# Optimization experiments

Measured on AMD Instinct MI355X. Metric: run time of the kernel, lower is better.

The kernel has to match this reference:

```python
import jax, jax.numpy as jnp
import numpy as np

B, S, D, H = 4, 2048, 1024, 16  # batch, seq, n_embd, n_head
HD = D // H  # head size = 64


def setup_inputs() -> dict:
    key = jax.random.key(0)
    ks = jax.random.split(key, 5)
    s = 0.02
    return {
        "x": jax.random.normal(ks[0], (B, S, D), dtype=jnp.float32),
        "W_attn": jax.random.normal(ks[1], (D, 3 * D), dtype=jnp.float32) * s,
        "b_attn": jnp.zeros((3 * D,), dtype=jnp.float32),
        "W_proj": jax.random.normal(ks[2], (D, D), dtype=jnp.float32) * s,
        "b_proj": jnp.zeros((D,), dtype=jnp.float32),
    }


def reference(x, W_attn, b_attn, W_proj, b_proj):
    Bx, Sx, Dx = x.shape
    qkv = x @ W_attn + b_attn  # [B,S,3D]
    q, k, v = jnp.split(qkv, 3, axis=-1)
    # [B,H,S,hd]
    q = q.reshape(Bx, Sx, H, HD).transpose(0, 2, 1, 3)
    k = k.reshape(Bx, Sx, H, HD).transpose(0, 2, 1, 3)
    v = v.reshape(Bx, Sx, H, HD).transpose(0, 2, 1, 3)
    scale = 1.0 / jnp.sqrt(jnp.asarray(HD, dtype=x.dtype))
    att = jnp.einsum("bhqd,bhkd->bhqk", q, k) * scale  # [B,H,S,S]
    causal = jnp.tril(jnp.ones((Sx, Sx), dtype=bool))
    att = jnp.where(causal[None, None, :, :], att, jnp.asarray(-jnp.inf, dtype=att.dtype))
    att = jax.nn.softmax(att, axis=-1)
    y = jnp.einsum("bhqk,bhkd->bhqd", att, v)  # [B,H,S,hd]
    y = y.transpose(0, 2, 1, 3).reshape(Bx, Sx, Dx)
    return y @ W_proj + b_proj
```

## Files before the change

### kernel.cpp

```cpp
#include <hip/hip_runtime.h>
#include <math.h>

#define SEQ 2048
#define DIM 1024
#define NH 16
#define HD 64
#define QKV_LD 3072

typedef __attribute__((ext_vector_type(8))) __bf16 bf16x8;
typedef __attribute__((ext_vector_type(8))) unsigned short u16x8;
typedef __attribute__((ext_vector_type(4))) unsigned short u16x4;
typedef __attribute__((ext_vector_type(4))) float f32x4;

typedef unsigned int __attribute__((may_alias)) u32a;

__device__ __forceinline__ unsigned short f2b(float f) {
  unsigned int b = __builtin_bit_cast(unsigned int, f);
  return (unsigned short)((b + 0x7fffu + ((b >> 16) & 1u)) >> 16);
}

__device__ __forceinline__ void gload_lds16(const void* g, void* l) {
  __builtin_amdgcn_global_load_lds((const __attribute__((address_space(1))) void*)g,
                                   (__attribute__((address_space(3))) void*)l,
                                   16, 0, 0);
}

__device__ __forceinline__ bf16x8 ld_frag16(const unsigned short* p) {
  bf16x8 r;
  __builtin_memcpy(&r, __builtin_assume_aligned((void*)p, 16), 16);
  return r;
}

#define BARRIER_VM4()  asm volatile("s_waitcnt vmcnt(4)\ns_barrier" ::: "memory")
#define BARRIER_LGKM() asm volatile("s_waitcnt lgkmcnt(0)\ns_barrier" ::: "memory")
#define ISSUE_FENCE()  asm volatile("" ::: "memory")


__global__ void to_bf16_kernel(const float* __restrict__ x,
                               unsigned short* __restrict__ y, int n) {
  int i = (blockIdx.x * blockDim.x + threadIdx.x) * 4;
  if (i >= n) return;
  float4 v = *(const float4*)(x + i);
  u16x4 o;
  o.x = f2b(v.x); o.y = f2b(v.y); o.z = f2b(v.z); o.w = f2b(v.w);
  *(u16x4*)(y + i) = o;
}

__global__ void transpose_to_bf16_kernel(const float* __restrict__ W,
                                         unsigned short* __restrict__ WT,
                                         int K, int N) {
  __shared__ float tile[32][33];
  const int n0 = blockIdx.x * 32, k0 = blockIdx.y * 32;
  const int tx = threadIdx.x, ty = threadIdx.y;
  tile[ty][tx] = W[(size_t)(k0 + ty) * N + n0 + tx];
  __syncthreads();
  WT[(size_t)(n0 + ty) * K + k0 + tx] = f2b(tile[tx][ty]);
}


template <int OUT_F32>
__global__ __launch_bounds__(256, 2) void gemm_bt_kernel(
    const unsigned short* __restrict__ A,
    const unsigned short* __restrict__ BT,
    const float* __restrict__ bias,
    void* __restrict__ C, int M, int N, int K,
    int scale_cols, float scale_val) {
  __shared__ __align__(16) unsigned short As[3][128 * 32];
  __shared__ __align__(16) unsigned short Bs[3][128 * 32];

  const int tid = threadIdx.x;
  const int wave = tid >> 6;
  const int lane = tid & 63;
  const int quad = lane >> 4;
  const int l16 = lane & 15;
  const int m0 = blockIdx.y * 128;
  const int n0 = blockIdx.x * 128;
  const int wm = (wave >> 1) * 64;
  const int wn = (wave & 1) * 64;

  const int srow = lane >> 2;
  const int scol8 = (lane & 3) ^ (srow & 3);
  const size_t a_g0 = (size_t)(m0 + wave * 32 + srow) * K + scol8 * 8;
  const size_t a_g1 = a_g0 + (size_t)16 * K;
  const size_t b_g0 = (size_t)(n0 + wave * 32 + srow) * K + scol8 * 8;
  const size_t b_g1 = b_g0 + (size_t)16 * K;
  const int lds_o0 = wave * 1024;
  const int lds_o1 = wave * 1024 + 512;

  const int rdc = (quad ^ (l16 & 3)) * 8;

  f32x4 acc[4][4] = {};
  const int NT = K >> 5;

#define G_STAGE(kt_, buf_)                                                     \
  {                                                                            \
    const int _k0 = (kt_) << 5;                                                \
    gload_lds16(A + a_g0 + _k0, &As[buf_][lds_o0]);                            \
    gload_lds16(A + a_g1 + _k0, &As[buf_][lds_o1]);                            \
    gload_lds16(BT + b_g0 + _k0, &Bs[buf_][lds_o0]);                           \
    gload_lds16(BT + b_g1 + _k0, &Bs[buf_][lds_o1]);                           \
  }

  G_STAGE(0, 0);
  ISSUE_FENCE();
  G_STAGE(1, 1);
  BARRIER_VM4();

  for (int t = 0; t < NT; ++t) {
    const int pf = (t + 2 < NT) ? t + 2 : NT - 1;
    G_STAGE(pf, (t + 2) % 3);

    const unsigned short* la = As[t % 3];
    const unsigned short* lb = Bs[t % 3];
    bf16x8 af[4];
#pragma unroll
    for (int i = 0; i < 4; ++i)
      af[i] = ld_frag16(&la[(wm + i * 16 + l16) * 32 + rdc]);
#pragma unroll
    for (int ni = 0; ni < 4; ++ni) {
      const bf16x8 bf = ld_frag16(&lb[(wn + ni * 16 + l16) * 32 + rdc]);
#pragma unroll
      for (int mi = 0; mi < 4; ++mi)
        acc[mi][ni] = __builtin_amdgcn_mfma_f32_16x16x32_bf16(af[mi], bf,
                                                              acc[mi][ni], 0, 0, 0);
    }
    BARRIER_VM4();
  }

#pragma unroll
  for (int mi = 0; mi < 4; ++mi) {
#pragma unroll
    for (int ni = 0; ni < 4; ++ni) {
      const int col = n0 + wn + ni * 16 + l16;
      const int row = m0 + wm + mi * 16 + quad * 4;
      const float bv = bias[col];
      const float sv = (col < scale_cols) ? scale_val : 1.0f;
#pragma unroll
      for (int r = 0; r < 4; ++r) {
        float v = (acc[mi][ni][r] + bv) * sv;
        if (OUT_F32)
          ((float*)C)[(size_t)(row + r) * N + col] = v;
        else
          ((unsigned short*)C)[(size_t)(row + r) * N + col] = f2b(v);
      }
    }
  }
}


#define FA_PREFETCH(g_, via_, vib_)                                            \
  {                                                                            \
    const int _g = (g_);                                                       \
    const int _tg = (_g < kt) ? _g : 0;                                        \
    const unsigned short* _kg =                                                \
        base + (size_t)(_tg * 64 + ktok_l) * QKV_LD + DIM + h * HD + kchunk * 8; \
    gload_lds16(_kg, &Ks[_g % 3][0][w * 512]);                                 \
    gload_lds16(_kg + 32, &Ks[_g % 3][1][w * 512]);                            \
    const unsigned short* _vg =                                                \
        base + (size_t)(_tg * 64 + 2 * vk) * QKV_LD + 2 * DIM + h * HD + vc;   \
    via_ = *(const u16x8*)_vg;                                                 \
    vib_ = *(const u16x8*)(_vg + QKV_LD);                                      \
  }

#define VT_WRITE(va_, vb_)                                                     \
  {                                                                            \
    u32a* _V32 = (u32a*)Vt;                                                    \
    _Pragma("unroll") for (int j = 0; j < 8; ++j)                              \
      _V32[vwidx[j]] = (unsigned int)(va_)[j] | ((unsigned int)(vb_)[j] << 16);\
  }

#define FA_COMPUTE(i_, t_, kt_, qf_)                                           \
  {                                                                            \
    const unsigned short* _kb0 = &Ks[(i_) % 3][0][0];                          \
    const unsigned short* _kb1 = &Ks[(i_) % 3][1][0];                          \
    bf16x8 kf0[4], kf1[4], vf0[4], vf1[4];                                     \
    _Pragma("unroll") for (int ni = 0; ni < 4; ++ni) {                         \
      const int ro = (ni * 16 + l16) * 32 + ((quad ^ rsw) * 8);                \
      kf0[ni] = ld_frag16(_kb0 + ro);                                          \
      kf1[ni] = ld_frag16(_kb1 + ro);                                          \
      vf0[ni] = ld_frag16(&Vt[quad * 512 + vroff[ni]]);                        \
      vf1[ni] = ld_frag16(&Vt[(4 + quad) * 512 + vroff[ni]]);                  \
    }                                                                          \
    const int qloc = w * 16 + quad * 4;                                        \
    _Pragma("unroll") for (int m = 0; m < 2; ++m) {                            \
      if (!(m == 0 && (t_) == (kt_)-1)) {   \
        const bool diag = ((t_) == (kt_)-2 + m);                               \
        _Pragma("unroll") for (int ni = 0; ni < 4; ++ni) {                     \
          f32x4 a = {};                                                        \
          a = __builtin_amdgcn_mfma_f32_16x16x32_bf16(qf_[m][0], kf0[ni], a, 0, 0, 0); \
          a = __builtin_amdgcn_mfma_f32_16x16x32_bf16(qf_[m][1], kf1[ni], a, 0, 0, 0); \
          const int kloc = ni * 16 + l16;                                      \
          _Pragma("unroll") for (int r = 0; r < 4; ++r) {                      \
            float p = __builtin_amdgcn_exp2f(a[r]);                            \
            if (diag && kloc > qloc + r) p = 0.0f;                 \
            Ps[w][(quad * 4 + r) * 72 + kloc] =                                \
                (unsigned short)(__builtin_bit_cast(unsigned int, p) >> 16);   \
          }                                                                    \
        }                                                                      \
        _Pragma("unroll") for (int c = 0; c < 2; ++c) {                        \
          const bf16x8 pa = ld_frag16(&Ps[w][l16 * 72 + c * 32 + quad * 8]);   \
          _Pragma("unroll") for (int ni = 0; ni < 4; ++ni)                     \
            o[m][ni] = __builtin_amdgcn_mfma_f32_16x16x32_bf16(                \
                pa, c ? vf1[ni] : vf0[ni], o[m][ni], 0, 0, 0);                 \
          lacc[m] = __builtin_amdgcn_mfma_f32_16x16x32_bf16(pa, onesb,         \
                                                            lacc[m], 0, 0, 0);\
        }                                                                      \
      }                                                                        \
    }                                                                          \
  }

#define FA_ITER(i_, t_, kt_, qf_, pva, pvb, cva, cvb)                          \
  {                                                                            \
    FA_PREFETCH((i_) + 2, pva, pvb);                                           \
    FA_COMPUTE(i_, t_, kt_, qf_);                                              \
    BARRIER_VM4();                                                             \
    if ((i_) + 1 < (kt_)) {                                                    \
      VT_WRITE(cva, cvb);                                                      \
      BARRIER_LGKM();                                                          \
    }                                                                          \
  }

#define FA_EPILOGUE(q0_)                                                       \
  _Pragma("unroll") for (int m = 0; m < 2; ++m)                                \
  _Pragma("unroll") for (int r = 0; r < 4; ++r) {                              \
    const float lv = __shfl(lacc[m][r], quad << 4);                            \
    const float inv = 1.0f / lv;                                               \
    const int row = (q0_) + m * 64 + w * 16 + quad * 4 + r;                    \
    unsigned short* dst = yatt + (size_t)(b * SEQ + row) * DIM + h * HD + l16; \
    _Pragma("unroll") for (int ni = 0; ni < 4; ++ni)                           \
      dst[ni * 16] = f2b(o[m][ni][r] * inv);                                   \
  }

__global__ __launch_bounds__(256, 2) void flash_kernel(
    const unsigned short* __restrict__ qkv,
    unsigned short* __restrict__ yatt) {
  __shared__ unsigned short Ks[3][2][64 * 32];
  __shared__ __align__(16) unsigned short Vt[8 * 64 * 8];
  __shared__ __align__(16) unsigned short Ps[4][16 * 72];

  const int tid = threadIdx.x;
  const int w = tid >> 6;
  const int lane = tid & 63;
  const int quad = lane >> 4;
  const int l16 = lane & 15;

  const int bid = (int)blockIdx.x;
  const int qt = 15 - (bid >> 6);
  const int bh = bid & 63;
  const int b = bh >> 4;
  const int h = bh & 15;
  const int kt = 2 * qt + 2;
  const int q0 = qt * 128;

  const unsigned short* base = qkv + (size_t)b * SEQ * QKV_LD;

  const int ktok_l = w * 16 + (lane >> 2);
  const int ksw = (ktok_l ^ (ktok_l >> 2)) & 3;
  const int kchunk = (lane & 3) ^ ksw;
  const int rsw = (l16 ^ (l16 >> 2)) & 3;

  const int vk = tid >> 3;
  const int vc = (tid & 7) * 8;
  int vwidx[8];
#pragma unroll
  for (int j = 0; j < 8; ++j)
    vwidx[j] = (vk >> 2) * 256 + (vc | ((j + (vc >> 3)) & 7)) * 4 + (vk & 3);
  int vroff[4];
#pragma unroll
  for (int ni = 0; ni < 4; ++ni) {
    const int dim = ni * 16 + l16;
    vroff[ni] = ((dim & 56) | ((dim + (dim >> 3)) & 7)) * 8;
  }

  u16x8 ob = {};
  if (l16 == 0) {
#pragma unroll
    for (int j = 0; j < 8; ++j) ob[j] = 0x3F80;
  }
  const bf16x8 onesb = __builtin_bit_cast(bf16x8, ob);

  bf16x8 qf[2][2];
#pragma unroll
  for (int m = 0; m < 2; ++m) {
    const unsigned short* qa =
        base + (size_t)(q0 + m * 64 + w * 16 + l16) * QKV_LD + h * HD + quad * 8;
    qf[m][0] = *(const bf16x8*)qa;
    qf[m][1] = *(const bf16x8*)(qa + 32);
  }

  u16x8 va0, vb0, va1, vb1;
  ISSUE_FENCE();
  FA_PREFETCH(0, va0, vb0);
  ISSUE_FENCE();
  FA_PREFETCH(1, va1, vb1);
  BARRIER_VM4();
  VT_WRITE(va0, vb0);
  BARRIER_LGKM();

  f32x4 o[2][4] = {};
  f32x4 lacc[2] = {};

  for (int i = 0; i < kt; i += 2) {
    FA_ITER(i,     i,     kt, qf, va0, vb0, va1, vb1);
    FA_ITER(i + 1, i + 1, kt, qf, va1, vb1, va0, vb0);
  }
  FA_EPILOGUE(q0);
}


extern "C" void kernel_launch(void* const* d_in, const int* in_sizes, int n_in,
                              void* d_out, int out_size, void* d_ws, size_t ws_size,
                              hipStream_t stream) {
  const float* x  = (const float*)d_in[0];
  const float* Wa = (const float*)d_in[1];
  const float* ba = (const float*)d_in[2];
  const float* Wp = (const float*)d_in[3];
  const float* bp = (const float*)d_in[4];
  float* out = (float*)d_out;

  char* ws = (char*)d_ws;
  unsigned short* xb   = (unsigned short*)ws;
  unsigned short* WaT  = (unsigned short*)(ws + 16777216);
  unsigned short* WpT  = (unsigned short*)(ws + 23068672);
  unsigned short* qkv  = (unsigned short*)(ws + 25165824);
  unsigned short* yatt = (unsigned short*)(ws + 75497472);

  const int M = 4 * SEQ;
  const float qscale = 0.125f * 1.44269504089f;

  to_bf16_kernel<<<8192, 256, 0, stream>>>(x, xb, M * DIM);
  transpose_to_bf16_kernel<<<dim3(96, 32), dim3(32, 32), 0, stream>>>(Wa, WaT, DIM, 3 * DIM);
  transpose_to_bf16_kernel<<<dim3(32, 32), dim3(32, 32), 0, stream>>>(Wp, WpT, DIM, DIM);

  gemm_bt_kernel<0><<<dim3(24, 64), 256, 0, stream>>>(xb, WaT, ba, qkv, M, 3 * DIM, DIM,
                                                      DIM, qscale);

  flash_kernel<<<dim3(1024), 256, 0, stream>>>(qkv, yatt);

  gemm_bt_kernel<1><<<dim3(8, 64), 256, 0, stream>>>(yatt, WpT, bp, out, M, DIM, DIM,
                                                     0, 1.0f);
}
```

Baseline: 262.8 us.

## Enlarge GEMM tiles to 256x128x64 with 8 waves and phased prefetch

The bf16 GEMM used for the QKV and output projections now uses a 256x128 block tile with a K-step of 64, 512 threads (8 waves) and an 8-way XOR-swizzled LDS layout. Each K-tile is split into two phases, and each phase issues part of the next stage's global-to-LDS loads before its MFMA batch. The MFMA sections in both the GEMM and the flash kernel are raised with s_setprio. The aim is more data reuse per LDS load, fewer barriers per FLOP and better overlap of loads with matrix math. In exchange the GEMM needs about 147KB of LDS per block, which limits occupancy to one block per CU.

```diff
diff --git a/kernel.cpp b/kernel.cpp
--- a/kernel.cpp
+++ b/kernel.cpp
@@ -32,7 +32,10 @@
 }
 
 #define BARRIER_VM4()  asm volatile("s_waitcnt vmcnt(4)\ns_barrier" ::: "memory")
+#define BARRIER_VM6()  asm volatile("s_waitcnt vmcnt(6)\ns_barrier" ::: "memory")
 #define BARRIER_LGKM() asm volatile("s_waitcnt lgkmcnt(0)\ns_barrier" ::: "memory")
+#define PH_BAR()       asm volatile("s_barrier" ::: "memory")
+#define LGKM0()        asm volatile("s_waitcnt lgkmcnt(0)" ::: "memory")
 #define ISSUE_FENCE()  asm volatile("" ::: "memory")
 
 
@@ -59,72 +62,83 @@
 
 
 template <int OUT_F32>
-__global__ __launch_bounds__(256, 2) void gemm_bt_kernel(
+__global__ __launch_bounds__(512, 2) void gemm_bt_v4_kernel(
     const unsigned short* __restrict__ A,
     const unsigned short* __restrict__ BT,
     const float* __restrict__ bias,
     void* __restrict__ C, int M, int N, int K,
     int scale_cols, float scale_val) {
-  __shared__ __align__(16) unsigned short As[3][128 * 32];
-  __shared__ __align__(16) unsigned short Bs[3][128 * 32];
+  __shared__ __align__(16) unsigned short As[3][256 * 64];
+  __shared__ __align__(16) unsigned short Bs[3][128 * 64];
 
   const int tid = threadIdx.x;
   const int wave = tid >> 6;
   const int lane = tid & 63;
   const int quad = lane >> 4;
   const int l16 = lane & 15;
-  const int m0 = blockIdx.y * 128;
+  const int r7 = l16 & 7;
+  const int m0 = blockIdx.y * 256;
   const int n0 = blockIdx.x * 128;
   const int wm = (wave >> 1) * 64;
   const int wn = (wave & 1) * 64;
 
-  const int srow = lane >> 2;
-  const int scol8 = (lane & 3) ^ (srow & 3);
-  const size_t a_g0 = (size_t)(m0 + wave * 32 + srow) * K + scol8 * 8;
-  const size_t a_g1 = a_g0 + (size_t)16 * K;
-  const size_t b_g0 = (size_t)(n0 + wave * 32 + srow) * K + scol8 * 8;
-  const size_t b_g1 = b_g0 + (size_t)16 * K;
-  const int lds_o0 = wave * 1024;
-  const int lds_o1 = wave * 1024 + 512;
-
-  const int rdc = (quad ^ (l16 & 3)) * 8;
+  const int srow = tid >> 3;
+  const int sg = (tid & 7) ^ (srow & 7);
+  const size_t a_gb = (size_t)(m0 + srow) * K + sg * 8;
+  const size_t b_gb = (size_t)(n0 + srow) * K + sg * 8;
 
   f32x4 acc[4][4] = {};
-  const int NT = K >> 5;
-
-#define G_STAGE(kt_, buf_)                                                     \
-  {                                                                            \
-    const int _k0 = (kt_) << 5;                                                \
-    gload_lds16(A + a_g0 + _k0, &As[buf_][lds_o0]);                            \
-    gload_lds16(A + a_g1 + _k0, &As[buf_][lds_o1]);                            \
-    gload_lds16(BT + b_g0 + _k0, &Bs[buf_][lds_o0]);                           \
-    gload_lds16(BT + b_g1 + _k0, &Bs[buf_][lds_o1]);                           \
-  }
-
-  G_STAGE(0, 0);
+  const int NT = K >> 6;
+
+#define G_STAGE_A(kt_, buf_, j_)                                               \
+  gload_lds16(A + a_gb + (size_t)(j_) * 64 * K + (size_t)(kt_) * 64,           \
+              &As[buf_][(j_) * 4096 + wave * 512])
+#define G_STAGE_B(kt_, buf_, j_)                                               \
+  gload_lds16(BT + b_gb + (size_t)(j_) * 64 * K + (size_t)(kt_) * 64,          \
+              &Bs[buf_][(j_) * 4096 + wave * 512])
+#define G_STAGE_ALL(kt_, buf_)                                                 \
+  {                                                                            \
+    G_STAGE_A(kt_, buf_, 0); G_STAGE_A(kt_, buf_, 1);                          \
+    G_STAGE_A(kt_, buf_, 2); G_STAGE_A(kt_, buf_, 3);                          \
+    G_STAGE_B(kt_, buf_, 0); G_STAGE_B(kt_, buf_, 1);                          \
+  }
+
+#define V4_PHASE(kk_, la_, lb_, STAGES_, BAR_)                                 \
+  {                                                                            \
+    const int colg = ((((kk_) << 2) | quad) ^ r7) << 3;                        \
+    bf16x8 af[4], bfr[4];                                                      \
+    _Pragma("unroll") for (int i = 0; i < 4; ++i)                              \
+      af[i] = ld_frag16(&(la_)[(wm + i * 16 + l16) * 64 + colg]);              \
+    _Pragma("unroll") for (int i = 0; i < 4; ++i)                              \
+      bfr[i] = ld_frag16(&(lb_)[(wn + i * 16 + l16) * 64 + colg]);             \
+    STAGES_;                                                                   \
+    BAR_;                                                                      \
+    LGKM0();                                                                   \
+    __builtin_amdgcn_s_setprio(1);                                             \
+    _Pragma("unroll") for (int ni = 0; ni < 4; ++ni)                           \
+      _Pragma("unroll") for (int mi = 0; mi < 4; ++mi)                         \
+        acc[mi][ni] = __builtin_amdgcn_mfma_f32_16x16x32_bf16(                 \
+            af[mi], bfr[ni], acc[mi][ni], 0, 0, 0);                            \
+    __builtin_amdgcn_s_setprio(0);                                             \
+    PH_BAR();                                                                  \
+  }
+
+  G_STAGE_ALL(0, 0);
   ISSUE_FENCE();
-  G_STAGE(1, 1);
-  BARRIER_VM4();
+  G_STAGE_ALL(1, 1);
+  BARRIER_VM6();
 
   for (int t = 0; t < NT; ++t) {
     const int pf = (t + 2 < NT) ? t + 2 : NT - 1;
-    G_STAGE(pf, (t + 2) % 3);
-
+    const int pb = (t + 2) % 3;
     const unsigned short* la = As[t % 3];
     const unsigned short* lb = Bs[t % 3];
-    bf16x8 af[4];
-#pragma unroll
-    for (int i = 0; i < 4; ++i)
-      af[i] = ld_frag16(&la[(wm + i * 16 + l16) * 32 + rdc]);
-#pragma unroll
-    for (int ni = 0; ni < 4; ++ni) {
-      const bf16x8 bf = ld_frag16(&lb[(wn + ni * 16 + l16) * 32 + rdc]);
-#pragma unroll
-      for (int mi = 0; mi < 4; ++mi)
-        acc[mi][ni] = __builtin_amdgcn_mfma_f32_16x16x32_bf16(af[mi], bf,
-                                                              acc[mi][ni], 0, 0, 0);
-    }
-    BARRIER_VM4();
+    V4_PHASE(0, la, lb,
+             { G_STAGE_A(pf, pb, 0); G_STAGE_A(pf, pb, 1); G_STAGE_B(pf, pb, 0); },
+             PH_BAR());
+    V4_PHASE(1, la, lb,
+             { G_STAGE_A(pf, pb, 2); G_STAGE_A(pf, pb, 3); G_STAGE_B(pf, pb, 1); },
+             BARRIER_VM6());
   }
 
 #pragma unroll
@@ -182,6 +196,7 @@
       vf1[ni] = ld_frag16(&Vt[(4 + quad) * 512 + vroff[ni]]);                  \
     }                                                                          \
     const int qloc = w * 16 + quad * 4;                                        \
+    __builtin_amdgcn_s_setprio(1);                                             \
     _Pragma("unroll") for (int m = 0; m < 2; ++m) {                            \
       if (!(m == 0 && (t_) == (kt_)-1)) {   \
         const bool diag = ((t_) == (kt_)-2 + m);                               \
@@ -207,6 +222,7 @@
         }                                                                      \
       }                                                                        \
     }                                                                          \
+    __builtin_amdgcn_s_setprio(0);                                             \
   }
 
 #define FA_ITER(i_, t_, kt_, qf_, pva, pvb, cva, cvb)                          \
@@ -332,11 +348,11 @@
   transpose_to_bf16_kernel<<<dim3(96, 32), dim3(32, 32), 0, stream>>>(Wa, WaT, DIM, 3 * DIM);
   transpose_to_bf16_kernel<<<dim3(32, 32), dim3(32, 32), 0, stream>>>(Wp, WpT, DIM, DIM);
 
-  gemm_bt_kernel<0><<<dim3(24, 64), 256, 0, stream>>>(xb, WaT, ba, qkv, M, 3 * DIM, DIM,
-                                                      DIM, qscale);
+  gemm_bt_v4_kernel<0><<<dim3(24, 32), 512, 0, stream>>>(xb, WaT, ba, qkv, M, 3 * DIM, DIM,
+                                                         DIM, qscale);
 
   flash_kernel<<<dim3(1024), 256, 0, stream>>>(qkv, yatt);
 
-  gemm_bt_kernel<1><<<dim3(8, 64), 256, 0, stream>>>(yatt, WpT, bp, out, M, DIM, DIM,
-                                                     0, 1.0f);
-}
+  gemm_bt_v4_kernel<1><<<dim3(8, 32), 512, 0, stream>>>(yatt, WpT, bp, out, M, DIM, DIM,
+                                                        0, 1.0f);
+}
```

New measurement: 250.5 us. 4.7% less time.
